# Optimization experiments

Hardware: AMD Instinct MI355X
Metric: run time of the kernel (lower is better)

## Reference

```python
import jax, jax.numpy as jnp
import numpy as np

N = 100000   # nodes
E = 1600000  # edges (avg degree 16)
D = 128      # feature width (constant across the 3 blocks)
L = 3        # number of residual LEConv blocks
EPS = 1e-5
SLOPE = 0.01  # leaky_relu negative slope


def setup_inputs() -> dict:
    key = jax.random.key(0)
    ks = jax.random.split(key, 10)
    y = jax.random.normal(ks[0], (N, D), dtype=jnp.float32)
    edge_index = jax.random.randint(ks[1], (2, E), 0, N, dtype=jnp.int64)
    s = 0.05
    W1 = jax.random.normal(ks[2], (L, D, D), dtype=jnp.float32) * s
    b1 = jax.random.normal(ks[3], (L, D), dtype=jnp.float32) * s
    W2 = jax.random.normal(ks[4], (L, D, D), dtype=jnp.float32) * s   # lin2: no bias
    W3 = jax.random.normal(ks[5], (L, D, D), dtype=jnp.float32) * s
    b3 = jax.random.normal(ks[6], (L, D), dtype=jnp.float32) * s
    ln_w = jnp.ones((L, D), dtype=jnp.float32)
    ln_b = jnp.zeros((L, D), dtype=jnp.float32)
    return {"y": y, "edge_index": edge_index, "W1": W1, "b1": b1,
            "W2": W2, "W3": W3, "b3": b3, "ln_w": ln_w, "ln_b": ln_b}


def reference(y, edge_index, W1, b1, W2, W3, b3, ln_w, ln_b):
    n = y.shape[0]
    src, dst = edge_index[0], edge_index[1]
    # in-degree per destination node (edge_weight = 1)
    deg = jax.ops.segment_sum(jnp.ones((src.shape[0],), dtype=y.dtype), dst,
                              num_segments=n)  # [N]
    for l in range(L):
        # LEConv: out_i = sum_{j->i} (lin1(x)_j - lin2(x)_i) + lin3(x)_i
        a = y @ W1[l] + b1[l]          # [N, D] (lin1, with bias)
        b = y @ W2[l]                  # [N, D] (lin2, no bias)
        agg = jax.ops.segment_sum(a[src], dst, num_segments=n) - deg[:, None] * b
        h = agg + y @ W3[l] + b3[l]    # + lin3(x)
        # PyG LayerNorm mode='graph', batch=None: scalar mean/std over all elems
        h = h - h.mean()
        h = h / (h.std() + EPS)
        h = h * ln_w[l] + ln_b[l]
        # leaky_relu, dropout p=0 (no-op), identity residual
        h = jnp.where(h >= 0, h, SLOPE * h)
        y = y + h
    return y
```

## Files before the change

### kernel.cpp

```cpp
#include <hip/hip_runtime.h>
#include <hip/hip_bf16.h>
#include <math.h>

#define N_NODES 100000
#define N_EDGES 1600000
#define DF      128
#define EPSV    1e-5f
#define SLOPE   0.01f
#define M_TOT   (N_NODES * DF)
#define NB_SCAN 391

typedef __hip_bfloat16 bf16;
typedef __attribute__((ext_vector_type(8))) short short8;
typedef __attribute__((ext_vector_type(4))) float f32x4;

__global__ void k_detect(const unsigned int* __restrict__ yw32, int* __restrict__ flagp)
{
    __shared__ int cnt;
    if (threadIdx.x == 0) cnt = 0;
    __syncthreads();
    unsigned w = yw32[threadIdx.x];
    int e = (w >> 7) & 0xFF;
    if (e >= 96 && e <= 140) atomicAdd(&cnt, 1);
    __syncthreads();
    if (threadIdx.x == 0) flagp[0] = (cnt >= 150) ? 1 : 0;
}

__global__ void k_zero(int* __restrict__ p, int n)
{
    int i = blockIdx.x * 256 + threadIdx.x;
    if (i < n) p[i] = 0;
}

__device__ __forceinline__ void edge_decode(const int* __restrict__ ei, int e,
                                            int& s, int& d)
{
    bool is64 = ((ei[1] | ei[3] | ei[5] | ei[7]) == 0);
    if (is64) { s = ei[2 * e]; d = ei[2 * (N_EDGES + e)]; }
    else      { s = ei[e];     d = ei[N_EDGES + e];       }
}

__global__ __launch_bounds__(256) void k_degcvt(
    const void* __restrict__ yin, bf16* __restrict__ yw,
    const int* __restrict__ flagp, const int* __restrict__ ei,
    int* __restrict__ degS, int* __restrict__ rank)
{
    const long t = (long)blockIdx.x * 256 + threadIdx.x;

    const int e = (int)t;
    int s, d;
    edge_decode(ei, e, s, d);
    const bool eok = ((unsigned)s < N_NODES) && ((unsigned)d < N_NODES);
    int r = 0;
    if (eok) r = atomicAdd(&degS[(size_t)d * 16], 1);

    const int isbf = flagp[0];
    float f[8];
    if (isbf) {
        uint4 v = reinterpret_cast<const uint4*>(yin)[t];
        const bf16* sp = reinterpret_cast<const bf16*>(&v);
#pragma unroll
        for (int j = 0; j < 8; ++j) f[j] = __bfloat162float(sp[j]);
    } else {
        float4 v0 = reinterpret_cast<const float4*>(yin)[2 * t];
        float4 v1 = reinterpret_cast<const float4*>(yin)[2 * t + 1];
        f[0] = v0.x; f[1] = v0.y; f[2] = v0.z; f[3] = v0.w;
        f[4] = v1.x; f[5] = v1.y; f[6] = v1.z; f[7] = v1.w;
    }
    uint4 ov;
    bf16* o = reinterpret_cast<bf16*>(&ov);
#pragma unroll
    for (int j = 0; j < 8; ++j) {
        float x = f[j];
        if (!isfinite(x)) x = 0.f;
        o[j] = __float2bfloat16(x);
    }
    reinterpret_cast<uint4*>(yw)[t] = ov;

    if (eok) rank[e] = r;
}

__global__ void k_compact(const int* __restrict__ degS, int* __restrict__ degcnt)
{
    int i = blockIdx.x * 256 + threadIdx.x;
    if (i < N_NODES) degcnt[i] = degS[(size_t)i * 16];
}

__global__ void k_wt(const void* __restrict__ W1, const void* __restrict__ W2,
                     const void* __restrict__ W3, bf16* __restrict__ Wt,
                     const int* __restrict__ flagp)
{
    int idx = blockIdx.x * 256 + threadIdx.x;
    const int isbf = flagp[0];
    int mat = idx >> 14;
    int r   = idx & 16383;
    int k   = r >> 7, n = r & 127;
    int l = mat / 3, which = mat - l * 3;
    const void* src = (which == 0) ? W1 : (which == 1 ? W2 : W3);
    size_t ofs = (size_t)l * 16384 + (size_t)k * 128 + n;
    float v = isbf ? __bfloat162float(reinterpret_cast<const bf16*>(src)[ofs])
                   : reinterpret_cast<const float*>(src)[ofs];
    if (!isfinite(v)) v = 0.f;
    Wt[((size_t)mat << 14) + (size_t)n * 128 + k] = __float2bfloat16(v);
}

__global__ void k_small(const void* __restrict__ b1, const void* __restrict__ b3,
                        const void* __restrict__ lnw, const void* __restrict__ lnb,
                        bf16* __restrict__ prm, const int* __restrict__ flagp)
{
    int i = blockIdx.x * 256 + threadIdx.x;
    if (i >= 1536) return;
    const int isbf = flagp[0];
    int which = i / 384, r = i - which * 384;
    const void* src = (which == 0) ? b1 : (which == 1) ? b3 : (which == 2) ? lnw : lnb;
    float v = isbf ? __bfloat162float(reinterpret_cast<const bf16*>(src)[r])
                   : reinterpret_cast<const float*>(src)[r];
    if (!isfinite(v)) v = 0.f;
    prm[i] = __float2bfloat16(v);
}

__global__ void k_scan1(const int* __restrict__ deg, int* __restrict__ bsum)
{
    __shared__ int red[4];
    int i = blockIdx.x * 256 + threadIdx.x;
    int v = (i < N_NODES) ? deg[i] : 0;
#pragma unroll
    for (int m = 1; m < 64; m <<= 1) v += __shfl_xor(v, m);
    if ((threadIdx.x & 63) == 0) red[threadIdx.x >> 6] = v;
    __syncthreads();
    if (threadIdx.x == 0) bsum[blockIdx.x] = red[0] + red[1] + red[2] + red[3];
}

__global__ void k_scan2(const int* __restrict__ bsum, int* __restrict__ bpre)
{
    __shared__ int sc[512];
    int tid = threadIdx.x;
    int v = (tid < NB_SCAN) ? bsum[tid] : 0;
    sc[tid] = v;
    __syncthreads();
    for (int off = 1; off < 512; off <<= 1) {
        int t = (tid >= off) ? sc[tid - off] : 0;
        __syncthreads();
        sc[tid] += t;
        __syncthreads();
    }
    if (tid < NB_SCAN) bpre[tid] = sc[tid] - v;
}

__global__ void k_scan3(const int* __restrict__ deg, const int* __restrict__ bpre,
                        int* __restrict__ offs)
{
    __shared__ int sc[256];
    int tid = threadIdx.x;
    int i = blockIdx.x * 256 + tid;
    int v = (i < N_NODES) ? deg[i] : 0;
    sc[tid] = v;
    __syncthreads();
    for (int off = 1; off < 256; off <<= 1) {
        int t = (tid >= off) ? sc[tid - off] : 0;
        __syncthreads();
        sc[tid] += t;
        __syncthreads();
    }
    if (i < N_NODES) offs[i] = bpre[blockIdx.x] + sc[tid] - v;
}

__global__ void k_fill(const int* __restrict__ ei, const int* __restrict__ offs,
                       const int* __restrict__ rank, int* __restrict__ edst)
{
    int e = blockIdx.x * 256 + threadIdx.x;
    if (e >= N_EDGES) return;
    int s, d;
    edge_decode(ei, e, s, d);
    if ((unsigned)s >= N_NODES || (unsigned)d >= N_NODES) return;
    edst[offs[d] + rank[e]] = s;
}

__global__ __launch_bounds__(256) void k_gemm3(
    bf16* __restrict__ yw, const bf16* __restrict__ hprev,
    const float* __restrict__ stats, const bf16* __restrict__ Wt,
    const bf16* __restrict__ prm, const int* __restrict__ degcnt,
    bf16* __restrict__ aBuf, bf16* __restrict__ cmb, int layer)
{
    __shared__ bf16 Asm[64][136];
    __shared__ bf16 Bsm[128][136];

    const int tid = threadIdx.x;
    const long r0 = (long)blockIdx.x * 64;

    const uint4* gy = reinterpret_cast<const uint4*>(yw);

    if (layer == 0) {
#pragma unroll
        for (int it = 0; it < 4; ++it) {
            int chunk = it * 256 + tid;
            int row = chunk >> 4, colc = (chunk & 15) * 8;
            uint4 v = make_uint4(0, 0, 0, 0);
            long grow = r0 + row;
            if (grow < N_NODES) v = gy[grow * 16 + (chunk & 15)];
            *reinterpret_cast<uint4*>(&Asm[row][colc]) = v;
        }
    } else {
        const float mean = stats[(layer - 1) * 2];
        const float inv  = stats[(layer - 1) * 2 + 1];
        const bf16* lnwc = prm + 768  + (layer - 1) * 128;
        const bf16* lnbc = prm + 1152 + (layer - 1) * 128;
        const uint4* gh = reinterpret_cast<const uint4*>(hprev);
#pragma unroll
        for (int it = 0; it < 4; ++it) {
            int chunk = it * 256 + tid;
            int row = chunk >> 4, c16 = chunk & 15, colc = c16 * 8;
            long grow = r0 + row;
            uint4 ov = make_uint4(0, 0, 0, 0);
            if (grow < N_NODES) {
                uint4 hv = gh[grow * 16 + c16];
                uint4 yv = gy[grow * 16 + c16];
                const bf16* h8 = reinterpret_cast<const bf16*>(&hv);
                const bf16* y8 = reinterpret_cast<const bf16*>(&yv);
                bf16* o8 = reinterpret_cast<bf16*>(&ov);
#pragma unroll
                for (int jj = 0; jj < 8; ++jj) {
                    float g = __bfloat162float(lnwc[colc + jj]);
                    float b = __bfloat162float(lnbc[colc + jj]);
                    float hh = (__bfloat162float(h8[jj]) - mean) * inv * g + b;
                    hh = (hh >= 0.f) ? hh : SLOPE * hh;
                    o8[jj] = __float2bfloat16(__bfloat162float(y8[jj]) + hh);
                }
                reinterpret_cast<uint4*>(yw)[grow * 16 + c16] = ov;
            }
            *reinterpret_cast<uint4*>(&Asm[row][colc]) = ov;
        }
    }

#define STAGE_B(MATIDX)                                                          \
    {                                                                            \
        const uint4* gw = reinterpret_cast<const uint4*>(Wt + ((size_t)(MATIDX) << 14)); \
        _Pragma("unroll")                                                        \
        for (int it = 0; it < 8; ++it) {                                         \
            int chunk = it * 256 + tid;                                          \
            *reinterpret_cast<uint4*>(&Bsm[chunk >> 4][(chunk & 15) * 8]) = gw[chunk]; \
        }                                                                        \
    }

    const int wave = tid >> 6, lane = tid & 63;
    const int lm = lane & 15, quad = lane >> 4;
    const int mrow = wave * 16 + lm;

    f32x4 accB[8], accC[8];
#pragma unroll
    for (int nt = 0; nt < 8; ++nt) {
        accB[nt] = (f32x4){0.f, 0.f, 0.f, 0.f};
        accC[nt] = (f32x4){0.f, 0.f, 0.f, 0.f};
    }

    STAGE_B(layer * 3 + 1);
    __syncthreads();
#pragma unroll
    for (int kk = 0; kk < 4; ++kk) {
        const int kb = kk * 32 + quad * 8;
        short8 afr = *reinterpret_cast<const short8*>(&Asm[mrow][kb]);
#pragma unroll
        for (int nt = 0; nt < 8; ++nt) {
            short8 bfr = *reinterpret_cast<const short8*>(&Bsm[nt * 16 + lm][kb]);
            accB[nt] = __builtin_amdgcn_mfma_f32_16x16x32_bf16(afr, bfr, accB[nt], 0, 0, 0);
        }
    }
    __syncthreads();

    STAGE_B(layer * 3 + 2);
    __syncthreads();
#pragma unroll
    for (int kk = 0; kk < 4; ++kk) {
        const int kb = kk * 32 + quad * 8;
        short8 afr = *reinterpret_cast<const short8*>(&Asm[mrow][kb]);
#pragma unroll
        for (int nt = 0; nt < 8; ++nt) {
            short8 bfr = *reinterpret_cast<const short8*>(&Bsm[nt * 16 + lm][kb]);
            accC[nt] = __builtin_amdgcn_mfma_f32_16x16x32_bf16(afr, bfr, accC[nt], 0, 0, 0);
        }
    }

    const bf16* b3c = prm + 384 + layer * 128;
#pragma unroll
    for (int i = 0; i < 4; ++i) {
        long row = r0 + wave * 16 + quad * 4 + i;
        if (row < N_NODES) {
            float degf = (float)degcnt[row];
#pragma unroll
            for (int nt = 0; nt < 8; ++nt) {
                int col = nt * 16 + lm;
                float v = accC[nt][i] + __bfloat162float(b3c[col]) - degf * accB[nt][i];
                cmb[row * 128 + col] = __float2bfloat16(v);
            }
        }
    }
    __syncthreads();

    STAGE_B(layer * 3 + 0);
    __syncthreads();
#pragma unroll
    for (int nt = 0; nt < 8; ++nt) accB[nt] = (f32x4){0.f, 0.f, 0.f, 0.f};
#pragma unroll
    for (int kk = 0; kk < 4; ++kk) {
        const int kb = kk * 32 + quad * 8;
        short8 afr = *reinterpret_cast<const short8*>(&Asm[mrow][kb]);
#pragma unroll
        for (int nt = 0; nt < 8; ++nt) {
            short8 bfr = *reinterpret_cast<const short8*>(&Bsm[nt * 16 + lm][kb]);
            accB[nt] = __builtin_amdgcn_mfma_f32_16x16x32_bf16(afr, bfr, accB[nt], 0, 0, 0);
        }
    }
    const bf16* b1c = prm + layer * 128;
#pragma unroll
    for (int i = 0; i < 4; ++i) {
        long row = r0 + wave * 16 + quad * 4 + i;
        if (row < N_NODES) {
#pragma unroll
            for (int nt = 0; nt < 8; ++nt) {
                int col = nt * 16 + lm;
                aBuf[row * 128 + col] =
                    __float2bfloat16(accB[nt][i] + __bfloat162float(b1c[col]));
            }
        }
    }
#undef STAGE_B
}

#define AGG_BLOCKS 2048
#define AGG_WAVES  (AGG_BLOCKS * 4)

__global__ __launch_bounds__(256, 8) void k_agg(
    const bf16* __restrict__ aBuf, bf16* __restrict__ cmb,
    const int* __restrict__ offs, const int* __restrict__ degcnt,
    const int* __restrict__ edst, float* __restrict__ buckets, int layer)
{
    const int tid  = threadIdx.x;
    const int lane = tid & 63;
    const int el   = lane >> 4;
    const int fb   = lane & 15;
    const int wid  = __builtin_amdgcn_readfirstlane((int)(blockIdx.x * 4) + (tid >> 6));

    const uint4* A4 = reinterpret_cast<const uint4*>(aBuf);

    float s1w = 0.f, s2w = 0.f;

#define ACC8(v)                                                                \
    {                                                                          \
        const unsigned* _u = reinterpret_cast<const unsigned*>(&(v));          \
        _Pragma("unroll")                                                      \
        for (int _d = 0; _d < 4; ++_d) {                                       \
            acc[2 * _d]     += __uint_as_float(_u[_d] << 16);                  \
            acc[2 * _d + 1] += __uint_as_float(_u[_d] & 0xffff0000u);          \
        }                                                                      \
    }

    for (int node = wid; node < N_NODES; node += AGG_WAVES) {
        const int start = offs[node];
        const int deg   = degcnt[node];

        const uint4 cv = reinterpret_cast<const uint4*>(cmb)[(size_t)node * 16 + fb];

        float acc[8];
#pragma unroll
        for (int i = 0; i < 8; ++i) acc[i] = 0.f;

        int j = el;
        for (; j + 12 < deg; j += 16) {
            int e0 = edst[start + j];
            int e1 = edst[start + j + 4];
            int e2 = edst[start + j + 8];
            int e3 = edst[start + j + 12];
            uint4 v0 = A4[(size_t)e0 * 16 + fb];
            uint4 v1 = A4[(size_t)e1 * 16 + fb];
            uint4 v2 = A4[(size_t)e2 * 16 + fb];
            uint4 v3 = A4[(size_t)e3 * 16 + fb];
            ACC8(v0); ACC8(v1); ACC8(v2); ACC8(v3);
        }
        if (j + 4 < deg) {
            int e0 = edst[start + j];
            int e1 = edst[start + j + 4];
            uint4 v0 = A4[(size_t)e0 * 16 + fb];
            uint4 v1 = A4[(size_t)e1 * 16 + fb];
            ACC8(v0); ACC8(v1);
            j += 8;
        }
        if (j < deg) {
            int e0 = edst[start + j];
            uint4 v0 = A4[(size_t)e0 * 16 + fb];
            ACC8(v0);
        }

#pragma unroll
        for (int i = 0; i < 8; ++i) {
            acc[i] += __shfl_xor(acc[i], 16);
            acc[i] += __shfl_xor(acc[i], 32);
        }

        const unsigned* cu = reinterpret_cast<const unsigned*>(&cv);
        float h[8];
#pragma unroll
        for (int d = 0; d < 4; ++d) {
            h[2 * d]     = acc[2 * d]     + __uint_as_float(cu[d] << 16);
            h[2 * d + 1] = acc[2 * d + 1] + __uint_as_float(cu[d] & 0xffff0000u);
        }
        uint4 ov;
        bf16* o8 = reinterpret_cast<bf16*>(&ov);
#pragma unroll
        for (int i = 0; i < 8; ++i) {
            o8[i] = __float2bfloat16(h[i]);
            s1w += h[i];
            s2w += h[i] * h[i];
        }
        if (el == 0) reinterpret_cast<uint4*>(cmb)[(size_t)node * 16 + fb] = ov;
    }
#undef ACC8

#pragma unroll
    for (int m = 1; m < 16; m <<= 1) {
        s1w += __shfl_xor(s1w, m);
        s2w += __shfl_xor(s2w, m);
    }
    if (lane == 0) {
        int bkt = wid & 255;
        atomicAdd(&buckets[layer * 512 + bkt * 2],     s1w);
        atomicAdd(&buckets[layer * 512 + bkt * 2 + 1], s2w);
    }
}

__global__ void k_red(const float* __restrict__ buckets, float* __restrict__ statsOut, int layer)
{
    __shared__ double red[8];
    const int tid = threadIdx.x;
    double s1 = (double)buckets[layer * 512 + tid * 2];
    double s2 = (double)buckets[layer * 512 + tid * 2 + 1];
#pragma unroll
    for (int m = 1; m < 64; m <<= 1) {
        s1 += __shfl_xor(s1, m);
        s2 += __shfl_xor(s2, m);
    }
    const int wv = tid >> 6;
    if ((tid & 63) == 0) { red[wv] = s1; red[4 + wv] = s2; }
    __syncthreads();
    if (tid == 0) {
        double S1 = red[0] + red[1] + red[2] + red[3];
        double S2 = red[4] + red[5] + red[6] + red[7];
        double mean, inv;
        if (isfinite(S1) && isfinite(S2)) {
            const double M = (double)M_TOT;
            mean = S1 / M;
            double var = S2 / M - mean * mean;
            if (!(var > 0.0)) var = 0.0;
            inv = 1.0 / (sqrt(var) + (double)EPSV);
        } else {
            mean = 0.0; inv = 1.0;
        }
        statsOut[layer * 2]     = (float)mean;
        statsOut[layer * 2 + 1] = (float)inv;
    }
}

__global__ __launch_bounds__(256) void k_norm(
    const bf16* __restrict__ hBuf, bf16* __restrict__ yw,
    const float* __restrict__ statsOut, const bf16* __restrict__ prm,
    void* __restrict__ outFinal, const int* __restrict__ flagp, int layer)
{
    const long i = (long)blockIdx.x * 256 + threadIdx.x;
    const float mean  = statsOut[layer * 2];
    const float scale = statsOut[layer * 2 + 1];

    uint4 hv = reinterpret_cast<const uint4*>(hBuf)[i];
    uint4 yv = reinterpret_cast<const uint4*>(yw)[i];
    const bf16* h8 = reinterpret_cast<const bf16*>(&hv);
    const bf16* y8 = reinterpret_cast<const bf16*>(&yv);
    const int colb = ((int)(i & 15)) * 8;
    const bf16* lnwc = prm + 768  + layer * 128;
    const bf16* lnbc = prm + 1152 + layer * 128;

    float r[8];
    uint4 ov;
    bf16* o8 = reinterpret_cast<bf16*>(&ov);
#pragma unroll
    for (int jj = 0; jj < 8; ++jj) {
        float g = __bfloat162float(lnwc[colb + jj]);
        float b = __bfloat162float(lnbc[colb + jj]);
        float h = (__bfloat162float(h8[jj]) - mean) * scale * g + b;
        h = (h >= 0.f) ? h : SLOPE * h;
        r[jj] = __bfloat162float(y8[jj]) + h;
        o8[jj] = __float2bfloat16(r[jj]);
    }
    if (flagp[0]) {
        reinterpret_cast<uint4*>(outFinal)[i] = ov;
    } else {
        float4 lo = make_float4(r[0], r[1], r[2], r[3]);
        float4 hi = make_float4(r[4], r[5], r[6], r[7]);
        reinterpret_cast<float4*>(outFinal)[2 * i]     = lo;
        reinterpret_cast<float4*>(outFinal)[2 * i + 1] = hi;
    }
}

extern "C" void kernel_launch(void* const* d_in, const int* in_sizes, int n_in,
                              void* d_out, int out_size, void* d_ws, size_t ws_size,
                              hipStream_t stream)
{
    const void* yIn = d_in[0];
    const int*  ei  = (const int*)d_in[1];
    const void* W1  = d_in[2];
    const void* b1  = d_in[3];
    const void* W2  = d_in[4];
    const void* W3  = d_in[5];
    const void* b3  = d_in[6];
    const void* lnw = d_in[7];
    const void* lnb = d_in[8];

    char* ws = (char*)d_ws;
    size_t o = 0;
    auto alloc = [&](size_t bytes) -> char* {
        char* p = ws + o;
        o += (bytes + 255) & ~(size_t)255;
        return p;
    };
    bf16* yw   = (bf16*)alloc((size_t)M_TOT * 2);
    bf16* aBuf = (bf16*)alloc((size_t)M_TOT * 2);
    bf16* cmb  = (bf16*)alloc((size_t)M_TOT * 2);
    bf16* Wt   = (bf16*)alloc((size_t)9 * 16384 * 2);
    bf16* prm  = (bf16*)alloc((size_t)1536 * 2);
    int*  edst = (int*)alloc((size_t)N_EDGES * 4);
    int*  rank = (int*)alloc((size_t)N_EDGES * 4);
    int*  offs = (int*)alloc((size_t)N_NODES * 4);
    int*  bsum = (int*)alloc((size_t)NB_SCAN * 4);
    int*  bpre = (int*)alloc((size_t)NB_SCAN * 4);
    const int nz = N_NODES + 3 * 512 + 8 + 8;
    int* zr = (int*)alloc((size_t)nz * 4);
    int*   degcnt   = zr;
    float* buckets  = (float*)(zr + N_NODES);
    float* statsOut = (float*)(zr + N_NODES + 3 * 512);
    int*   flagp    = zr + N_NODES + 3 * 512 + 8;

    int* degS = (int*)aBuf;

    const int nS = N_NODES * 16;
    k_zero   <<<(nS + 255) / 256, 256, 0, stream>>>(degS, nS);
    k_zero   <<<(nz + 255) / 256, 256, 0, stream>>>(zr, nz);
    k_detect <<<1, 256, 0, stream>>>((const unsigned int*)yIn, flagp);
    k_degcvt <<<N_EDGES / 256, 256, 0, stream>>>(yIn, yw, flagp, ei, degS, rank);
    k_compact<<<NB_SCAN, 256, 0, stream>>>(degS, degcnt);
    k_wt     <<<(9 * 16384) / 256, 256, 0, stream>>>(W1, W2, W3, Wt, flagp);
    k_small  <<<6, 256, 0, stream>>>(b1, b3, lnw, lnb, prm, flagp);
    k_scan1  <<<NB_SCAN, 256, 0, stream>>>(degcnt, bsum);
    k_scan2  <<<1, 512, 0, stream>>>(bsum, bpre);
    k_scan3  <<<NB_SCAN, 256, 0, stream>>>(degcnt, bpre, offs);
    k_fill   <<<N_EDGES / 256, 256, 0, stream>>>(ei, offs, rank, edst);

    const int ngemm = (N_NODES + 63) / 64;
    for (int l = 0; l < 3; ++l) {
        k_gemm3<<<ngemm, 256, 0, stream>>>(yw, cmb, statsOut, Wt, prm, degcnt, aBuf, cmb, l);
        k_agg  <<<AGG_BLOCKS, 256, 0, stream>>>(aBuf, cmb, offs, degcnt, edst, buckets, l);
        k_red  <<<1, 256, 0, stream>>>(buckets, statsOut, l);
    }
    k_norm<<<M_TOT / (8 * 256), 256, 0, stream>>>(cmb, yw, statsOut, prm, d_out, flagp, 2);
}
```

Baseline: 538.8 us.

## Build CSR via two-level binned counting sort instead of global atomics

Replaces the global-atomic degree counting, padded degree array, rank buffer and three-pass scan with a two-level counting sort. Edges are first histogrammed per 256-node bin in shared memory and scattered into bin order, then each bin is sorted by node locally with shared atomics. This removes contended global atomics and the large zeroed padded degree buffer, at the cost of an extra pass over edges and a bin-packed intermediate. The y conversion becomes grid-stride inside the histogram kernel.

```diff
diff --git a/kernel.cpp b/kernel.cpp
--- a/kernel.cpp
+++ b/kernel.cpp
@@ -8,7 +8,10 @@
 #define EPSV    1e-5f
 #define SLOPE   0.01f
 #define M_TOT   (N_NODES * DF)
-#define NB_SCAN 391
+
+#define HG    512
+#define EPB   (N_EDGES / HG)
+#define NBIN  391
 
 typedef __hip_bfloat16 bf16;
 typedef __attribute__((ext_vector_type(8))) short short8;
@@ -40,50 +43,153 @@
     else      { s = ei[e];     d = ei[N_EDGES + e];       }
 }
 
-__global__ __launch_bounds__(256) void k_degcvt(
+__global__ __launch_bounds__(256) void k_hist(
     const void* __restrict__ yin, bf16* __restrict__ yw,
     const int* __restrict__ flagp, const int* __restrict__ ei,
-    int* __restrict__ degS, int* __restrict__ rank)
-{
-    const long t = (long)blockIdx.x * 256 + threadIdx.x;
-
-    const int e = (int)t;
-    int s, d;
-    edge_decode(ei, e, s, d);
-    const bool eok = ((unsigned)s < N_NODES) && ((unsigned)d < N_NODES);
-    int r = 0;
-    if (eok) r = atomicAdd(&degS[(size_t)d * 16], 1);
+    int* __restrict__ histG)
+{
+    __shared__ int h[NBIN];
+    const int tid = threadIdx.x, b = blockIdx.x;
+    for (int i = tid; i < NBIN; i += 256) h[i] = 0;
+    __syncthreads();
+
+    const int e0 = b * EPB;
+    for (int e = e0 + tid; e < e0 + EPB; e += 256) {
+        int s, d;
+        edge_decode(ei, e, s, d);
+        if ((unsigned)s < N_NODES && (unsigned)d < N_NODES)
+            atomicAdd(&h[d >> 8], 1);
+    }
 
     const int isbf = flagp[0];
-    float f[8];
-    if (isbf) {
-        uint4 v = reinterpret_cast<const uint4*>(yin)[t];
-        const bf16* sp = reinterpret_cast<const bf16*>(&v);
-#pragma unroll
-        for (int j = 0; j < 8; ++j) f[j] = __bfloat162float(sp[j]);
-    } else {
-        float4 v0 = reinterpret_cast<const float4*>(yin)[2 * t];
-        float4 v1 = reinterpret_cast<const float4*>(yin)[2 * t + 1];
-        f[0] = v0.x; f[1] = v0.y; f[2] = v0.z; f[3] = v0.w;
-        f[4] = v1.x; f[5] = v1.y; f[6] = v1.z; f[7] = v1.w;
-    }
-    uint4 ov;
-    bf16* o = reinterpret_cast<bf16*>(&ov);
-#pragma unroll
-    for (int j = 0; j < 8; ++j) {
-        float x = f[j];
-        if (!isfinite(x)) x = 0.f;
-        o[j] = __float2bfloat16(x);
-    }
-    reinterpret_cast<uint4*>(yw)[t] = ov;
-
-    if (eok) rank[e] = r;
-}
-
-__global__ void k_compact(const int* __restrict__ degS, int* __restrict__ degcnt)
-{
-    int i = blockIdx.x * 256 + threadIdx.x;
-    if (i < N_NODES) degcnt[i] = degS[(size_t)i * 16];
+    for (long t = (long)b * 256 + tid; t < (M_TOT / 8); t += (long)HG * 256) {
+        float f[8];
+        if (isbf) {
+            uint4 v = reinterpret_cast<const uint4*>(yin)[t];
+            const bf16* sp = reinterpret_cast<const bf16*>(&v);
+#pragma unroll
+            for (int j = 0; j < 8; ++j) f[j] = __bfloat162float(sp[j]);
+        } else {
+            float4 v0 = reinterpret_cast<const float4*>(yin)[2 * t];
+            float4 v1 = reinterpret_cast<const float4*>(yin)[2 * t + 1];
+            f[0] = v0.x; f[1] = v0.y; f[2] = v0.z; f[3] = v0.w;
+            f[4] = v1.x; f[5] = v1.y; f[6] = v1.z; f[7] = v1.w;
+        }
+        uint4 ov;
+        bf16* o = reinterpret_cast<bf16*>(&ov);
+#pragma unroll
+        for (int j = 0; j < 8; ++j) {
+            float x = f[j];
+            if (!isfinite(x)) x = 0.f;
+            o[j] = __float2bfloat16(x);
+        }
+        reinterpret_cast<uint4*>(yw)[t] = ov;
+    }
+
+    __syncthreads();
+    for (int i = tid; i < NBIN; i += 256) histG[i * HG + b] = h[i];
+}
+
+__global__ void k_hscan1(int* __restrict__ histG, int* __restrict__ binTotal)
+{
+    __shared__ int sc[512];
+    const int bin = blockIdx.x, tid = threadIdx.x;
+    int v = histG[bin * HG + tid];
+    sc[tid] = v;
+    __syncthreads();
+    for (int off = 1; off < 512; off <<= 1) {
+        int t = (tid >= off) ? sc[tid - off] : 0;
+        __syncthreads();
+        sc[tid] += t;
+        __syncthreads();
+    }
+    histG[bin * HG + tid] = sc[tid] - v;
+    if (tid == 511) binTotal[bin] = sc[511];
+}
+
+__global__ void k_hscan2(const int* __restrict__ binTotal, int* __restrict__ binStart)
+{
+    __shared__ int sc[512];
+    int tid = threadIdx.x;
+    int v = (tid < NBIN) ? binTotal[tid] : 0;
+    sc[tid] = v;
+    __syncthreads();
+    for (int off = 1; off < 512; off <<= 1) {
+        int t = (tid >= off) ? sc[tid - off] : 0;
+        __syncthreads();
+        sc[tid] += t;
+        __syncthreads();
+    }
+    if (tid < NBIN) binStart[tid] = sc[tid] - v;
+}
+
+__global__ __launch_bounds__(256) void k_scatter(
+    const int* __restrict__ ei, const int* __restrict__ histG,
+    const int* __restrict__ binStart, int* __restrict__ binned)
+{
+    __shared__ int base[NBIN];
+    __shared__ int cur[NBIN];
+    const int tid = threadIdx.x, b = blockIdx.x;
+    for (int i = tid; i < NBIN; i += 256) {
+        base[i] = binStart[i] + histG[i * HG + b];
+        cur[i]  = 0;
+    }
+    __syncthreads();
+
+    const int e0 = b * EPB;
+    for (int e = e0 + tid; e < e0 + EPB; e += 256) {
+        int s, d;
+        edge_decode(ei, e, s, d);
+        if ((unsigned)s < N_NODES && (unsigned)d < N_NODES) {
+            int bin = d >> 8;
+            int r = atomicAdd(&cur[bin], 1);
+            binned[base[bin] + r] = ((d & 255) << 17) | s;
+        }
+    }
+}
+
+__global__ __launch_bounds__(256) void k_bin(
+    const int* __restrict__ binned, const int* __restrict__ binStart,
+    const int* __restrict__ binTotal, int* __restrict__ edst,
+    int* __restrict__ degcnt, int* __restrict__ offs)
+{
+    __shared__ int hloc[256];
+    __shared__ int lofs[256];
+    __shared__ int sc[256];
+    const int bin = blockIdx.x, tid = threadIdx.x;
+    const int bbase = binStart[bin], cnt = binTotal[bin];
+
+    hloc[tid] = 0;
+    __syncthreads();
+    for (int i = tid; i < cnt; i += 256)
+        atomicAdd(&hloc[binned[bbase + i] >> 17], 1);
+    __syncthreads();
+
+    const int deg = hloc[tid];
+    sc[tid] = deg;
+    __syncthreads();
+    for (int off = 1; off < 256; off <<= 1) {
+        int t = (tid >= off) ? sc[tid - off] : 0;
+        __syncthreads();
+        sc[tid] += t;
+        __syncthreads();
+    }
+    const int ex = sc[tid] - deg;
+    lofs[tid] = ex;
+    const int node = bin * 256 + tid;
+    if (node < N_NODES) {
+        degcnt[node] = deg;
+        offs[node]   = bbase + ex;
+    }
+    hloc[tid] = 0;
+    __syncthreads();
+
+    for (int i = tid; i < cnt; i += 256) {
+        int v = binned[bbase + i];
+        int n = v >> 17;
+        int r = atomicAdd(&hloc[n], 1);
+        edst[bbase + lofs[n] + r] = v & 0x1FFFF;
+    }
 }
 
 __global__ void k_wt(const void* __restrict__ W1, const void* __restrict__ W2,
@@ -119,63 +225,6 @@
     prm[i] = __float2bfloat16(v);
 }
 
-__global__ void k_scan1(const int* __restrict__ deg, int* __restrict__ bsum)
-{
-    __shared__ int red[4];
-    int i = blockIdx.x * 256 + threadIdx.x;
-    int v = (i < N_NODES) ? deg[i] : 0;
-#pragma unroll
-    for (int m = 1; m < 64; m <<= 1) v += __shfl_xor(v, m);
-    if ((threadIdx.x & 63) == 0) red[threadIdx.x >> 6] = v;
-    __syncthreads();
-    if (threadIdx.x == 0) bsum[blockIdx.x] = red[0] + red[1] + red[2] + red[3];
-}
-
-__global__ void k_scan2(const int* __restrict__ bsum, int* __restrict__ bpre)
-{
-    __shared__ int sc[512];
-    int tid = threadIdx.x;
-    int v = (tid < NB_SCAN) ? bsum[tid] : 0;
-    sc[tid] = v;
-    __syncthreads();
-    for (int off = 1; off < 512; off <<= 1) {
-        int t = (tid >= off) ? sc[tid - off] : 0;
-        __syncthreads();
-        sc[tid] += t;
-        __syncthreads();
-    }
-    if (tid < NB_SCAN) bpre[tid] = sc[tid] - v;
-}
-
-__global__ void k_scan3(const int* __restrict__ deg, const int* __restrict__ bpre,
-                        int* __restrict__ offs)
-{
-    __shared__ int sc[256];
-    int tid = threadIdx.x;
-    int i = blockIdx.x * 256 + tid;
-    int v = (i < N_NODES) ? deg[i] : 0;
-    sc[tid] = v;
-    __syncthreads();
-    for (int off = 1; off < 256; off <<= 1) {
-        int t = (tid >= off) ? sc[tid - off] : 0;
-        __syncthreads();
-        sc[tid] += t;
-        __syncthreads();
-    }
-    if (i < N_NODES) offs[i] = bpre[blockIdx.x] + sc[tid] - v;
-}
-
-__global__ void k_fill(const int* __restrict__ ei, const int* __restrict__ offs,
-                       const int* __restrict__ rank, int* __restrict__ edst)
-{
-    int e = blockIdx.x * 256 + threadIdx.x;
-    if (e >= N_EDGES) return;
-    int s, d;
-    edge_decode(ei, e, s, d);
-    if ((unsigned)s >= N_NODES || (unsigned)d >= N_NODES) return;
-    edst[offs[d] + rank[e]] = s;
-}
-
 __global__ __launch_bounds__(256) void k_gemm3(
     bf16* __restrict__ yw, const bf16* __restrict__ hprev,
     const float* __restrict__ stats, const bf16* __restrict__ Wt,
@@ -519,37 +568,33 @@
         o += (bytes + 255) & ~(size_t)255;
         return p;
     };
-    bf16* yw   = (bf16*)alloc((size_t)M_TOT * 2);
-    bf16* aBuf = (bf16*)alloc((size_t)M_TOT * 2);
-    bf16* cmb  = (bf16*)alloc((size_t)M_TOT * 2);
-    bf16* Wt   = (bf16*)alloc((size_t)9 * 16384 * 2);
-    bf16* prm  = (bf16*)alloc((size_t)1536 * 2);
-    int*  edst = (int*)alloc((size_t)N_EDGES * 4);
-    int*  rank = (int*)alloc((size_t)N_EDGES * 4);
-    int*  offs = (int*)alloc((size_t)N_NODES * 4);
-    int*  bsum = (int*)alloc((size_t)NB_SCAN * 4);
-    int*  bpre = (int*)alloc((size_t)NB_SCAN * 4);
-    const int nz = N_NODES + 3 * 512 + 8 + 8;
+    bf16* yw     = (bf16*)alloc((size_t)M_TOT * 2);
+    bf16* aBuf   = (bf16*)alloc((size_t)M_TOT * 2);
+    bf16* cmb    = (bf16*)alloc((size_t)M_TOT * 2);
+    bf16* Wt     = (bf16*)alloc((size_t)9 * 16384 * 2);
+    bf16* prm    = (bf16*)alloc((size_t)1536 * 2);
+    int*  edst   = (int*)alloc((size_t)N_EDGES * 4);
+    int*  binned = (int*)alloc((size_t)N_EDGES * 4);
+    int*  histG  = (int*)alloc((size_t)NBIN * HG * 4);
+    int*  binTot = (int*)alloc((size_t)NBIN * 4);
+    int*  binSta = (int*)alloc((size_t)NBIN * 4);
+    int*  offs   = (int*)alloc((size_t)N_NODES * 4);
+    int*  degcnt = (int*)alloc((size_t)N_NODES * 4);
+    const int nz = 3 * 512 + 8 + 8;
     int* zr = (int*)alloc((size_t)nz * 4);
-    int*   degcnt   = zr;
-    float* buckets  = (float*)(zr + N_NODES);
-    float* statsOut = (float*)(zr + N_NODES + 3 * 512);
-    int*   flagp    = zr + N_NODES + 3 * 512 + 8;
-
-    int* degS = (int*)aBuf;
-
-    const int nS = N_NODES * 16;
-    k_zero   <<<(nS + 255) / 256, 256, 0, stream>>>(degS, nS);
+    float* buckets  = (float*)zr;
+    float* statsOut = (float*)(zr + 3 * 512);
+    int*   flagp    = zr + 3 * 512 + 8;
+
     k_zero   <<<(nz + 255) / 256, 256, 0, stream>>>(zr, nz);
     k_detect <<<1, 256, 0, stream>>>((const unsigned int*)yIn, flagp);
-    k_degcvt <<<N_EDGES / 256, 256, 0, stream>>>(yIn, yw, flagp, ei, degS, rank);
-    k_compact<<<NB_SCAN, 256, 0, stream>>>(degS, degcnt);
+    k_hist   <<<HG, 256, 0, stream>>>(yIn, yw, flagp, ei, histG);
+    k_hscan1 <<<NBIN, 512, 0, stream>>>(histG, binTot);
+    k_hscan2 <<<1, 512, 0, stream>>>(binTot, binSta);
+    k_scatter<<<HG, 256, 0, stream>>>(ei, histG, binSta, binned);
+    k_bin    <<<NBIN, 256, 0, stream>>>(binned, binSta, binTot, edst, degcnt, offs);
     k_wt     <<<(9 * 16384) / 256, 256, 0, stream>>>(W1, W2, W3, Wt, flagp);
     k_small  <<<6, 256, 0, stream>>>(b1, b3, lnw, lnb, prm, flagp);
-    k_scan1  <<<NB_SCAN, 256, 0, stream>>>(degcnt, bsum);
-    k_scan2  <<<1, 512, 0, stream>>>(bsum, bpre);
-    k_scan3  <<<NB_SCAN, 256, 0, stream>>>(degcnt, bpre, offs);
-    k_fill   <<<N_EDGES / 256, 256, 0, stream>>>(ei, offs, rank, edst);
 
     const int ngemm = (N_NODES + 63) / 64;
     for (int l = 0; l < 3; ++l) {
```

After: 492.9 us. -8.5%, faster.
